# Kernel tuning notes

Measured on AMD Instinct MI355X. Metric: run time of the kernel, lower is better.

## Reference

```python
import jax, jax.numpy as jnp
import numpy as np

H = 12  # num_heads


def rotate_half(x):
    x1, x2 = jnp.split(x, 2, axis=-1)
    return jnp.concatenate([-x2, x1], axis=-1)


def setup_inputs() -> dict:
    key = jax.random.key(0)
    ks = jax.random.split(key, 8)
    B, N, C = 4, 2048, 768
    num_special = 5
    Ns = N - num_special
    D = C // H
    x = jax.random.normal(ks[0], (B, N, C), dtype=jnp.float32)
    rope_cos = jax.random.uniform(ks[1], (Ns, D), dtype=jnp.float32)
    rope_sin = jax.random.uniform(ks[2], (Ns, D), dtype=jnp.float32)
    W_qkv = jax.random.normal(ks[3], (C, 3 * C), dtype=jnp.float32) * (C ** -0.5)
    b_qkv = jax.random.normal(ks[4], (3 * C,), dtype=jnp.float32) * 0.02
    W_proj = jax.random.normal(ks[5], (C, C), dtype=jnp.float32) * (C ** -0.5)
    b_proj = jax.random.normal(ks[6], (C,), dtype=jnp.float32) * 0.02
    return {"x": x, "rope_cos": rope_cos, "rope_sin": rope_sin,
            "W_qkv": W_qkv, "b_qkv": b_qkv, "W_proj": W_proj, "b_proj": b_proj,
            "num_special": num_special}


def reference(x, rope_cos, rope_sin, W_qkv, b_qkv, W_proj, b_proj, num_special):
    B, N, C = x.shape
    D = C // H
    scale = D ** -0.5
    qkv = (x @ W_qkv + b_qkv).reshape(B, N, 3, H, D)
    qkv = jnp.transpose(qkv, (2, 0, 3, 1, 4))  # [3, B, H, N, D]
    q, k, v = qkv[0], qkv[1], qkv[2]
    # partial RoPE: special tokens untouched, spatial tokens rotated
    q_spec, q_spat = q[:, :, :num_special], q[:, :, num_special:]
    k_spec, k_spat = k[:, :, :num_special], k[:, :, num_special:]
    q_spat = q_spat * rope_cos + rotate_half(q_spat) * rope_sin
    k_spat = k_spat * rope_cos + rotate_half(k_spat) * rope_sin
    q = jnp.concatenate([q_spec, q_spat], axis=2)
    k = jnp.concatenate([k_spec, k_spat], axis=2)
    attn = jnp.einsum('bhqd,bhkd->bhqk', q, k) * scale  # [B,H,N,N]
    attn = jax.nn.softmax(attn, axis=-1)
    out = jnp.einsum('bhqk,bhkd->bhqd', attn, v)  # [B,H,N,D]
    out = jnp.transpose(out, (0, 2, 1, 3)).reshape(B, N, C)
    return out @ W_proj + b_proj
```

## Files before the change

### kernel.cpp

```cpp
#include <hip/hip_runtime.h>
#include <stdint.h>

typedef unsigned short u16;
typedef __bf16 bf16x8 __attribute__((ext_vector_type(8)));
typedef __bf16 bf16x2 __attribute__((ext_vector_type(2)));
typedef short s16x4 __attribute__((ext_vector_type(4)));
typedef float f32x4 __attribute__((ext_vector_type(4)));

typedef __attribute__((address_space(1))) void gvoid_t;
typedef __attribute__((address_space(3))) void lvoid_t;

struct alignas(16) U128 { uint32_t x, y, z, w; };
struct alignas(16) F128 { float x, y, z, w; };
struct alignas(8)  U64v { uint32_t x, y; };

__device__ __forceinline__ void gld16(const u16* g, u16* lds) {
  __builtin_amdgcn_global_load_lds((gvoid_t*)const_cast<u16*>(g),
                                   (lvoid_t*)lds, 16, 0, 0);
}

__device__ __forceinline__ u16 f2bf(float f) {
  uint32_t u = __builtin_bit_cast(uint32_t, f);
  u += 0x7FFFu + ((u >> 16) & 1u);
  return (u16)(u >> 16);
}
__device__ __forceinline__ float bf2f(u16 h) {
  return __builtin_bit_cast(float, (uint32_t)h << 16);
}
__device__ __forceinline__ bf16x8 ldfrag(const u16* p) {
  U128 u = *reinterpret_cast<const U128*>(p);
  return __builtin_bit_cast(bf16x8, u);
}
__device__ __forceinline__ uint32_t pkbf(float a, float b) {
  bf16x2 v;
  v[0] = (__bf16)a;
  v[1] = (__bf16)b;
  return __builtin_bit_cast(uint32_t, v);
}

__device__ __forceinline__ float EXP2(float x) { return __builtin_amdgcn_exp2f(x); }

__global__ void cvt_f32_bf16(const float* __restrict__ in, u16* __restrict__ out) {
  int i = (blockIdx.x * 256 + threadIdx.x) * 4;
  F128 v = *reinterpret_cast<const F128*>(in + i);
  U64v o;
  o.x = (uint32_t)f2bf(v.x) | ((uint32_t)f2bf(v.y) << 16);
  o.y = (uint32_t)f2bf(v.z) | ((uint32_t)f2bf(v.w) << 16);
  *reinterpret_cast<U64v*>(out + i) = o;
}

__global__ void transpose_cvt(const float* __restrict__ W, u16* __restrict__ Wt,
                              int K, int N) {
  __shared__ float T[32][33];
  const int n0 = blockIdx.x * 32, k0 = blockIdx.y * 32;
  const int tid = threadIdx.x;
#pragma unroll
  for (int i = 0; i < 4; ++i) {
    int e = i * 256 + tid, r = e >> 5, c = e & 31;
    T[r][c] = W[(size_t)(k0 + r) * N + n0 + c];
  }
  __syncthreads();
#pragma unroll
  for (int i = 0; i < 4; ++i) {
    int e = i * 256 + tid, r = e >> 5, c = e & 31;
    Wt[(size_t)(n0 + r) * K + k0 + c] = f2bf(T[c][r]);
  }
}


#define GEMM_PIPE(A_, Bt_, KD_, NKT_)                                                \
  const int tid = threadIdx.x;                                                       \
  const int wave = tid >> 6, lane = tid & 63;                                        \
  const int quad = lane >> 4, l16 = lane & 15;                                       \
  const int m0 = by * 128, n0 = bx * 128;                                            \
  const int wr = (wave & 1) * 64, wc = (wave >> 1) * 64;                             \
  f32x4 acc[4][4];                                                                   \
  _Pragma("unroll")                                                                  \
  for (int i = 0; i < 4; ++i)                                                        \
    _Pragma("unroll")                                                                \
    for (int j = 0; j < 4; ++j) acc[i][j] = (f32x4){0.f, 0.f, 0.f, 0.f};             \
  const int c0 = wave * 128 + lane;                                                  \
  const int row0 = c0 >> 2, kq0 = c0 & 3;                                            \
  const int c1 = c0 + 64;                                                            \
  const int row1 = c1 >> 2, kq1 = c1 & 3;                                            \
  const u16* Ag0 = (A_) + (size_t)(m0 + row0) * (KD_) + kq0 * 8;                     \
  const u16* Ag1 = (A_) + (size_t)(m0 + row1) * (KD_) + kq1 * 8;                     \
  const u16* Bg0 = (Bt_) + (size_t)(n0 + row0) * (KD_) + kq0 * 8;                    \
  const u16* Bg1 = (Bt_) + (size_t)(n0 + row1) * (KD_) + kq1 * 8;                    \
  STG(0, 0);                                                                         \
  STG(1, 1);                                                                         \
  for (int t = 0; t < (NKT_); ++t) {                                                 \
    __builtin_amdgcn_sched_barrier(0);                                               \
    if (t < (NKT_) - 1) asm volatile("s_waitcnt vmcnt(4)" ::: "memory");             \
    else                asm volatile("s_waitcnt vmcnt(0)" ::: "memory");             \
    __builtin_amdgcn_sched_barrier(0);                                               \
    __builtin_amdgcn_s_barrier();                                                    \
    __builtin_amdgcn_sched_barrier(0);                                               \
    if (t + 2 < (NKT_)) STG(t + 2, (t + 2) % 3);                                     \
    const u16* Ab = Asl + (t % 3) * 4096;                                            \
    const u16* Bb = Bsl + (t % 3) * 4096;                                            \
    bf16x8 af[4], bfr[4];                                                            \
    _Pragma("unroll")                                                                \
    for (int rb = 0; rb < 4; ++rb)                                                   \
      af[rb] = ldfrag(&Ab[(wr + rb * 16 + l16) * 32 + quad * 8]);                    \
    _Pragma("unroll")                                                                \
    for (int cb = 0; cb < 4; ++cb)                                                   \
      bfr[cb] = ldfrag(&Bb[(wc + cb * 16 + l16) * 32 + quad * 8]);                   \
    __builtin_amdgcn_s_setprio(1);                                                   \
    _Pragma("unroll")                                                                \
    for (int rb = 0; rb < 4; ++rb)                                                   \
      _Pragma("unroll")                                                              \
      for (int cb = 0; cb < 4; ++cb)                                                 \
        acc[rb][cb] = __builtin_amdgcn_mfma_f32_16x16x32_bf16(                       \
            af[rb], bfr[cb], acc[rb][cb], 0, 0, 0);                                  \
    __builtin_amdgcn_s_setprio(0);                                                   \
  }

#define STG(t_, s_)                                                                  \
  do {                                                                               \
    const int k0_ = (t_) * 32;                                                       \
    gld16(Ag0 + k0_, &Asl[(s_) * 4096 + wave * 1024]);                               \
    gld16(Bg0 + k0_, &Bsl[(s_) * 4096 + wave * 1024]);                               \
    gld16(Ag1 + k0_, &Asl[(s_) * 4096 + wave * 1024 + 512]);                         \
    gld16(Bg1 + k0_, &Bsl[(s_) * 4096 + wave * 1024 + 512]);                         \
  } while (0)

__global__ __launch_bounds__(256, 3)
void gemm_bt(const u16* __restrict__ A, const u16* __restrict__ Bt,
             const float* __restrict__ bias, float* __restrict__ C,
             int M, int N, int Karg) {
  (void)M; (void)Karg;
  __shared__ u16 Asl[3 * 4096];
  __shared__ u16 Bsl[3 * 4096];
  const int orig = blockIdx.y * 6 + blockIdx.x;
  const int swz = (orig % 8) * 48 + orig / 8;
  const int bx = swz % 6, by = swz / 6;
  GEMM_PIPE(A, Bt, 768, 24)
#pragma unroll
  for (int cb = 0; cb < 4; ++cb) {
    int col = n0 + wc + cb * 16 + l16;
    float bv = bias[col];
#pragma unroll
    for (int rb = 0; rb < 4; ++rb) {
#pragma unroll
      for (int r = 0; r < 4; ++r) {
        int row = m0 + wr + rb * 16 + quad * 4 + r;
        C[(size_t)row * N + col] = acc[rb][cb][r] + bv;
      }
    }
  }
}

__global__ __launch_bounds__(256, 3)
void gemm_qkv_rope(const u16* __restrict__ A, const u16* __restrict__ Bt,
                   const float* __restrict__ bias,
                   const float* __restrict__ cosT, const float* __restrict__ sinT,
                   const int* __restrict__ nsp,
                   u16* __restrict__ Qo, u16* __restrict__ Ko, u16* __restrict__ Vto) {
  __shared__ u16 Asl[3 * 4096];
  __shared__ u16 Bsl[3 * 4096];
  const int orig = blockIdx.y * 18 + blockIdx.x;
  const int swz = (orig % 8) * 144 + orig / 8;
  const int bx = swz % 18, by = swz / 18;
  GEMM_PIPE(A, Bt, 768, 24)

  const int sec = bx / 6;
  const int gcol0 = n0 + wc;
  const int hh = (gcol0 >> 6) % 12;
  const int bb = m0 >> 11;
  const int nbase = m0 & 2047;
  const int bh = bb * 12 + hh;
  const int num_special = nsp[0];
  const float QS = 0.125f * 1.4426950408889634f;

  if (sec < 2) {
    u16* outp = sec ? Ko : Qo;
    const float qs = sec ? 1.0f : QS;
#pragma unroll
    for (int cbp = 0; cbp < 2; ++cbp) {
      const int d1 = cbp * 16 + l16;
      const int d2 = d1 + 32;
      const float bv1 = bias[gcol0 + d1];
      const float bv2 = bias[gcol0 + d2];
#pragma unroll
      for (int rb = 0; rb < 4; ++rb) {
#pragma unroll
        for (int r = 0; r < 4; ++r) {
          const int n = nbase + wr + rb * 16 + quad * 4 + r;
          float v1 = acc[rb][cbp][r] + bv1;
          float v2 = acc[rb][cbp + 2][r] + bv2;
          float o1, o2;
          if (n < num_special) {
            o1 = v1; o2 = v2;
          } else {
            int ns = n - num_special;
            float c1 = cosT[ns * 64 + d1], s1 = sinT[ns * 64 + d1];
            float c2 = cosT[ns * 64 + d2], s2 = sinT[ns * 64 + d2];
            o1 = v1 * c1 - v2 * s1;
            o2 = v2 * c2 + v1 * s2;
          }
          size_t ob = ((size_t)bh * 2048 + n) * 64;
          outp[ob + d1] = f2bf(o1 * qs);
          outp[ob + d2] = f2bf(o2 * qs);
        }
      }
    }
  } else {
#pragma unroll
    for (int cb = 0; cb < 4; ++cb) {
      const int d = cb * 16 + l16;
      const float bv = bias[gcol0 + d];
#pragma unroll
      for (int rb = 0; rb < 4; ++rb) {
        const int nr = nbase + wr + rb * 16 + quad * 4;
        U64v o;
        o.x = (uint32_t)f2bf(acc[rb][cb][0] + bv) |
              ((uint32_t)f2bf(acc[rb][cb][1] + bv) << 16);
        o.y = (uint32_t)f2bf(acc[rb][cb][2] + bv) |
              ((uint32_t)f2bf(acc[rb][cb][3] + bv) << 16);
        *(U64v*)&Vto[((size_t)bh * 64 + d) * 2048 + nr] = o;
      }
    }
  }
}

__global__ __launch_bounds__(256, 3)
void attn(const u16* __restrict__ Q, const u16* __restrict__ Kg,
          const u16* __restrict__ Vt, u16* __restrict__ Out, int qt0) {
  __shared__ u16 smem2[2 * 8192];
  __shared__ float invS[64];
  const int tid = threadIdx.x;
  const int wave = tid >> 6, lane = tid & 63;
  const int quad = lane >> 4, l16 = lane & 15;
  const int idx = blockIdx.x;
  const int bh = idx % 48, qt = idx / 48 + qt0;
  const int b = bh / 12, h = bh % 12;
  const u16* Qb = Q + (size_t)bh * 2048 * 64;
  const u16* Kb = Kg + (size_t)bh * 2048 * 64;
  const u16* Vb = Vt + (size_t)bh * 64 * 2048;
  const int wkey0 = wave * 16;

  const int lrow = lane >> 3;
  const int lch  = (lane & 7) ^ (lrow & 7);
  const int r0a = wave * 8;
  const int r0b = 32 + wave * 8;
  const int ksrc_a = (r0a + lrow) * 64 + lch * 8;
  const int ksrc_b = (r0b + lrow) * 64 + lch * 8;
  const size_t vsrc_a = (size_t)(r0a + lrow) * 2048 + lch * 8;
  const size_t vsrc_b = (size_t)(r0b + lrow) * 2048 + lch * 8;

  const int krd = (wkey0 + l16) * 64 + ((quad ^ (l16 & 7)) << 3);
  int vrd[4];
#pragma unroll
  for (int db = 0; db < 4; ++db)
    vrd[db] = (db * 16 + l16) * 64 +
              ((((wave << 1) | (quad >> 1)) ^ (l16 & 7)) << 3) + (quad & 1) * 4;

#define STAGE_A(kt_, s_)                                                      \
  do {                                                                        \
    u16* Kd = smem2 + (s_) * 8192;                                            \
    u16* Vd = Kd + 4096;                                                      \
    const u16* Ksrc = Kb + (size_t)(kt_) * 4096;                              \
    const u16* Vsrc = Vb + (kt_) * 64;                                        \
    gld16(Ksrc + ksrc_a, Kd + r0a * 64);                                      \
    gld16(Ksrc + ksrc_b, Kd + r0b * 64);                                      \
    gld16(Vsrc + vsrc_a, Vd + r0a * 64);                                      \
    gld16(Vsrc + vsrc_b, Vd + r0b * 64);                                      \
  } while (0)

  bf16x8 qf[4][2];
#pragma unroll
  for (int m = 0; m < 4; ++m) {
    const u16* qp = Qb + (size_t)(qt * 64 + m * 16 + l16) * 64 + quad * 8;
    qf[m][0] = ldfrag(qp);
    qf[m][1] = ldfrag(qp + 32);
  }

  f32x4 oacc[4][4];
#pragma unroll
  for (int m = 0; m < 4; ++m)
#pragma unroll
    for (int db = 0; db < 4; ++db) oacc[m][db] = (f32x4){0.f, 0.f, 0.f, 0.f};
  float psum[4] = {0.f, 0.f, 0.f, 0.f};

  STAGE_A(0, 0);
  STAGE_A(1, 1);
  __syncthreads();

  s16x4 pf[4];
  U64v  vfc[4];
  {
    const u16* Ksh = smem2;
    const u16* Vsh = smem2 + 4096;
    bf16x8 ka0 = ldfrag(Ksh + krd);
    bf16x8 ka1 = ldfrag(Ksh + (krd ^ 32));
#pragma unroll
    for (int db = 0; db < 4; ++db) vfc[db] = *(const U64v*)(Vsh + vrd[db]);
#pragma unroll
    for (int m = 0; m < 4; ++m) {
      f32x4 st = (f32x4){0.f, 0.f, 0.f, 0.f};
      st = __builtin_amdgcn_mfma_f32_16x16x32_bf16(ka0, qf[m][0], st, 0, 0, 0);
      st = __builtin_amdgcn_mfma_f32_16x16x32_bf16(ka1, qf[m][1], st, 0, 0, 0);
      float p0 = EXP2(st[0]), p1 = EXP2(st[1]), p2 = EXP2(st[2]), p3 = EXP2(st[3]);
      psum[m] += (p0 + p1) + (p2 + p3);
      U64v pd; pd.x = pkbf(p0, p1); pd.y = pkbf(p2, p3);
      pf[m] = __builtin_bit_cast(s16x4, pd);
    }
  }
  __syncthreads();

  for (int kt = 0; kt < 31; ++kt) {
    const int cur = kt & 1, nxt = cur ^ 1;
    const u16* Kshn = smem2 + nxt * 8192;
    const u16* Vshn = Kshn + 4096;
    bf16x8 kn0 = ldfrag(Kshn + krd);
    bf16x8 kn1 = ldfrag(Kshn + (krd ^ 32));
    U64v vfn[4];
#pragma unroll
    for (int db = 0; db < 4; ++db) vfn[db] = *(const U64v*)(Vshn + vrd[db]);

    if (kt < 30) STAGE_A(kt + 2, cur);

    s16x4 pfn[4];
#pragma unroll
    for (int m = 0; m < 4; ++m) {
      f32x4 st = (f32x4){0.f, 0.f, 0.f, 0.f};
      st = __builtin_amdgcn_mfma_f32_16x16x32_bf16(kn0, qf[m][0], st, 0, 0, 0);
      st = __builtin_amdgcn_mfma_f32_16x16x32_bf16(kn1, qf[m][1], st, 0, 0, 0);
#pragma unroll
      for (int db = 0; db < 4; ++db)
        oacc[m][db] = __builtin_amdgcn_mfma_f32_16x16x16bf16_1k(pf[m], __builtin_bit_cast(s16x4, vfc[db]), oacc[m][db], 0, 0, 0);
      float p0 = EXP2(st[0]), p1 = EXP2(st[1]), p2 = EXP2(st[2]), p3 = EXP2(st[3]);
      psum[m] += (p0 + p1) + (p2 + p3);
      U64v pd; pd.x = pkbf(p0, p1); pd.y = pkbf(p2, p3);
      pfn[m] = __builtin_bit_cast(s16x4, pd);
    }
    __syncthreads();
#pragma unroll
    for (int m = 0; m < 4; ++m) pf[m] = pfn[m];
#pragma unroll
    for (int db = 0; db < 4; ++db) vfc[db] = vfn[db];
  }

#pragma unroll
  for (int m = 0; m < 4; ++m)
#pragma unroll
    for (int db = 0; db < 4; ++db)
      oacc[m][db] = __builtin_amdgcn_mfma_f32_16x16x16bf16_1k(pf[m], __builtin_bit_cast(s16x4, vfc[db]), oacc[m][db], 0, 0, 0);
#undef STAGE_A

#pragma unroll
  for (int m = 0; m < 4; ++m) {
    psum[m] += __shfl_xor(psum[m], 16, 64);
    psum[m] += __shfl_xor(psum[m], 32, 64);
  }
  __syncthreads();
  float* LS = (float*)smem2;
  if (quad == 0) {
#pragma unroll
    for (int m = 0; m < 4; ++m) LS[wave * 64 + m * 16 + l16] = psum[m];
  }
  __syncthreads();
  if (tid < 64) {
    float tot = LS[tid] + LS[64 + tid] + LS[128 + tid] + LS[192 + tid];
    invS[tid] = 1.0f / tot;
  }

  float* OR = (float*)smem2;
  const int q = tid >> 2;
  const int d0 = (tid & 3) * 4;
  const size_t obase = ((size_t)(b * 2048 + qt * 64 + q)) * 768 + h * 64 + d0;
#pragma unroll
  for (int db = 0; db < 4; ++db) {
    __syncthreads();
#pragma unroll
    for (int m = 0; m < 4; ++m)
#pragma unroll
      for (int r = 0; r < 4; ++r)
        OR[(wave * 64 + m * 16 + quad * 4 + r) * 18 + l16] = oacc[m][db][r];
    __syncthreads();
    float s0 = 0.f, s1 = 0.f, s2 = 0.f, s3 = 0.f;
#pragma unroll
    for (int w = 0; w < 4; ++w) {
      const float* p = &OR[(w * 64 + q) * 18 + d0];
      s0 += p[0]; s1 += p[1]; s2 += p[2]; s3 += p[3];
    }
    float iv = invS[q];
    U64v o;
    o.x = (uint32_t)f2bf(s0 * iv) | ((uint32_t)f2bf(s1 * iv) << 16);
    o.y = (uint32_t)f2bf(s2 * iv) | ((uint32_t)f2bf(s3 * iv) << 16);
    *(U64v*)&Out[obase + db * 16] = o;
  }
}

extern "C" void kernel_launch(void* const* d_in, const int* in_sizes, int n_in,
                              void* d_out, int out_size, void* d_ws, size_t ws_size,
                              hipStream_t stream) {
  (void)in_sizes; (void)n_in; (void)out_size; (void)ws_size;
  const float* x        = (const float*)d_in[0];
  const float* rope_cos = (const float*)d_in[1];
  const float* rope_sin = (const float*)d_in[2];
  const float* W_qkv    = (const float*)d_in[3];
  const float* b_qkv    = (const float*)d_in[4];
  const float* W_proj   = (const float*)d_in[5];
  const float* b_proj   = (const float*)d_in[6];
  const int*   nsp      = (const int*)d_in[7];
  float* out = (float*)d_out;

  char* ws = (char*)d_ws;
  u16* Xb   = (u16*)(ws);
  u16* Wqkt = (u16*)(ws + 12582912);
  u16* Wpt  = (u16*)(ws + 16121856);
  u16* Qb   = (u16*)(ws + 55050240);
  u16* Kb   = (u16*)(ws + 67633152);
  u16* Vtb  = (u16*)(ws + 80216064);
  u16* att  = (u16*)(ws + 92798976);

  cvt_f32_bf16<<<6144, 256, 0, stream>>>(x, Xb);
  transpose_cvt<<<dim3(72, 24), 256, 0, stream>>>(W_qkv, Wqkt, 768, 2304);
  transpose_cvt<<<dim3(24, 24), 256, 0, stream>>>(W_proj, Wpt, 768, 768);
  gemm_qkv_rope<<<dim3(18, 64), 256, 0, stream>>>(Xb, Wqkt, b_qkv, rope_cos, rope_sin,
                                                  nsp, Qb, Kb, Vtb);
  attn<<<768, 256, 0, stream>>>(Qb, Kb, Vtb, att, 0);
  attn<<<768, 256, 0, stream>>>(Qb, Kb, Vtb, att, 16);
  gemm_bt<<<dim3(6, 64), 256, 0, stream>>>(att, Wpt, b_proj, out, 8192, 768, 768);
}
```

Measured before the change: 248.9 us.

## Pair key tiles so PV uses 16x16x32 MFMA and merge attention launches

The attention loop now processes two 64-key tiles per iteration and concatenates their P and V fragments, so the PV product uses the wider 16x16x32 bf16 MFMA instead of two 16x16x16 ones. This halves the PV MFMA instruction count. It also changes software pipelining, since PV for a pair is issued after both QK tiles, and holds more fragments in registers. The two attention launches are merged into one grid of 1536 blocks, removing a launch and a tail.

Measured after the change: 368.1 us. 1.48x slower.

```diff
diff --git a/kernel.cpp b/kernel.cpp
--- a/kernel.cpp
+++ b/kernel.cpp
@@ -29,6 +29,10 @@
 }
 __device__ __forceinline__ bf16x8 ldfrag(const u16* p) {
   U128 u = *reinterpret_cast<const U128*>(p);
+  return __builtin_bit_cast(bf16x8, u);
+}
+__device__ __forceinline__ bf16x8 cat8(U64v lo, U64v hi) {
+  U128 u; u.x = lo.x; u.y = lo.y; u.z = hi.x; u.w = hi.y;
   return __builtin_bit_cast(bf16x8, u);
 }
 __device__ __forceinline__ uint32_t pkbf(float a, float b) {
@@ -226,14 +230,14 @@
 
 __global__ __launch_bounds__(256, 3)
 void attn(const u16* __restrict__ Q, const u16* __restrict__ Kg,
-          const u16* __restrict__ Vt, u16* __restrict__ Out, int qt0) {
+          const u16* __restrict__ Vt, u16* __restrict__ Out) {
   __shared__ u16 smem2[2 * 8192];
   __shared__ float invS[64];
   const int tid = threadIdx.x;
   const int wave = tid >> 6, lane = tid & 63;
   const int quad = lane >> 4, l16 = lane & 15;
   const int idx = blockIdx.x;
-  const int bh = idx % 48, qt = idx / 48 + qt0;
+  const int bh = idx % 48, qt = idx / 48;
   const int b = bh / 12, h = bh % 12;
   const u16* Qb = Q + (size_t)bh * 2048 * 64;
   const u16* Kb = Kg + (size_t)bh * 2048 * 64;
@@ -268,6 +272,25 @@
     gld16(Vsrc + vsrc_b, Vd + r0b * 64);                                      \
   } while (0)
 
+#define QK_TILE(Ksh_, Vsh_, pf_, vdst_)                                       \
+  do {                                                                        \
+    bf16x8 ka0_ = ldfrag((Ksh_) + krd);                                       \
+    bf16x8 ka1_ = ldfrag((Ksh_) + (krd ^ 32));                                \
+    _Pragma("unroll")                                                         \
+    for (int db = 0; db < 4; ++db)                                            \
+      (vdst_)[db] = *(const U64v*)((Vsh_) + vrd[db]);                         \
+    _Pragma("unroll")                                                         \
+    for (int m = 0; m < 4; ++m) {                                             \
+      f32x4 st = (f32x4){0.f, 0.f, 0.f, 0.f};                                 \
+      st = __builtin_amdgcn_mfma_f32_16x16x32_bf16(ka0_, qf[m][0], st, 0, 0, 0); \
+      st = __builtin_amdgcn_mfma_f32_16x16x32_bf16(ka1_, qf[m][1], st, 0, 0, 0); \
+      float p0 = EXP2(st[0]), p1 = EXP2(st[1]), p2 = EXP2(st[2]), p3 = EXP2(st[3]); \
+      psum[m] += (p0 + p1) + (p2 + p3);                                       \
+      U64v pd_; pd_.x = pkbf(p0, p1); pd_.y = pkbf(p2, p3);                   \
+      (pf_)[m] = pd_;                                                         \
+    }                                                                         \
+  } while (0)
+
   bf16x8 qf[4][2];
 #pragma unroll
   for (int m = 0; m < 4; ++m) {
@@ -283,71 +306,56 @@
     for (int db = 0; db < 4; ++db) oacc[m][db] = (f32x4){0.f, 0.f, 0.f, 0.f};
   float psum[4] = {0.f, 0.f, 0.f, 0.f};
 
+  U64v pfE[4], pfO[4], vE[4], vO[4];
+
   STAGE_A(0, 0);
   STAGE_A(1, 1);
   __syncthreads();
-
-  s16x4 pf[4];
-  U64v  vfc[4];
+  QK_TILE(smem2, smem2 + 4096, pfE, vE);
+  __syncthreads();
+
+  for (int j = 0; j < 15; ++j) {
+    {
+      const u16* Ksh = smem2 + 8192;
+      STAGE_A(2 * j + 2, 0);
+      QK_TILE(Ksh, Ksh + 4096, pfO, vO);
+      __syncthreads();
+    }
+    {
+      const u16* Ksh = smem2;
+      U64v pfN[4], vN[4];
+      STAGE_A(2 * j + 3, 1);
+      QK_TILE(Ksh, Ksh + 4096, pfN, vN);
+#pragma unroll
+      for (int db = 0; db < 4; ++db) {
+        bf16x8 vf8 = cat8(vE[db], vO[db]);
+#pragma unroll
+        for (int m = 0; m < 4; ++m)
+          oacc[m][db] = __builtin_amdgcn_mfma_f32_16x16x32_bf16(
+              cat8(pfE[m], pfO[m]), vf8, oacc[m][db], 0, 0, 0);
+      }
+      __syncthreads();
+#pragma unroll
+      for (int m = 0; m < 4; ++m) pfE[m] = pfN[m];
+#pragma unroll
+      for (int db = 0; db < 4; ++db) vE[db] = vN[db];
+    }
+  }
+
   {
-    const u16* Ksh = smem2;
-    const u16* Vsh = smem2 + 4096;
-    bf16x8 ka0 = ldfrag(Ksh + krd);
-    bf16x8 ka1 = ldfrag(Ksh + (krd ^ 32));
-#pragma unroll
-    for (int db = 0; db < 4; ++db) vfc[db] = *(const U64v*)(Vsh + vrd[db]);
-#pragma unroll
-    for (int m = 0; m < 4; ++m) {
-      f32x4 st = (f32x4){0.f, 0.f, 0.f, 0.f};
-      st = __builtin_amdgcn_mfma_f32_16x16x32_bf16(ka0, qf[m][0], st, 0, 0, 0);
-      st = __builtin_amdgcn_mfma_f32_16x16x32_bf16(ka1, qf[m][1], st, 0, 0, 0);
-      float p0 = EXP2(st[0]), p1 = EXP2(st[1]), p2 = EXP2(st[2]), p3 = EXP2(st[3]);
-      psum[m] += (p0 + p1) + (p2 + p3);
-      U64v pd; pd.x = pkbf(p0, p1); pd.y = pkbf(p2, p3);
-      pf[m] = __builtin_bit_cast(s16x4, pd);
-    }
-  }
-  __syncthreads();
-
-  for (int kt = 0; kt < 31; ++kt) {
-    const int cur = kt & 1, nxt = cur ^ 1;
-    const u16* Kshn = smem2 + nxt * 8192;
-    const u16* Vshn = Kshn + 4096;
-    bf16x8 kn0 = ldfrag(Kshn + krd);
-    bf16x8 kn1 = ldfrag(Kshn + (krd ^ 32));
-    U64v vfn[4];
-#pragma unroll
-    for (int db = 0; db < 4; ++db) vfn[db] = *(const U64v*)(Vshn + vrd[db]);
-
-    if (kt < 30) STAGE_A(kt + 2, cur);
-
-    s16x4 pfn[4];
-#pragma unroll
-    for (int m = 0; m < 4; ++m) {
-      f32x4 st = (f32x4){0.f, 0.f, 0.f, 0.f};
-      st = __builtin_amdgcn_mfma_f32_16x16x32_bf16(kn0, qf[m][0], st, 0, 0, 0);
-      st = __builtin_amdgcn_mfma_f32_16x16x32_bf16(kn1, qf[m][1], st, 0, 0, 0);
-#pragma unroll
-      for (int db = 0; db < 4; ++db)
-        oacc[m][db] = __builtin_amdgcn_mfma_f32_16x16x16bf16_1k(pf[m], __builtin_bit_cast(s16x4, vfc[db]), oacc[m][db], 0, 0, 0);
-      float p0 = EXP2(st[0]), p1 = EXP2(st[1]), p2 = EXP2(st[2]), p3 = EXP2(st[3]);
-      psum[m] += (p0 + p1) + (p2 + p3);
-      U64v pd; pd.x = pkbf(p0, p1); pd.y = pkbf(p2, p3);
-      pfn[m] = __builtin_bit_cast(s16x4, pd);
-    }
-    __syncthreads();
-#pragma unroll
-    for (int m = 0; m < 4; ++m) pf[m] = pfn[m];
-#pragma unroll
-    for (int db = 0; db < 4; ++db) vfc[db] = vfn[db];
-  }
-
-#pragma unroll
-  for (int m = 0; m < 4; ++m)
-#pragma unroll
-    for (int db = 0; db < 4; ++db)
-      oacc[m][db] = __builtin_amdgcn_mfma_f32_16x16x16bf16_1k(pf[m], __builtin_bit_cast(s16x4, vfc[db]), oacc[m][db], 0, 0, 0);
+    const u16* Ksh = smem2 + 8192;
+    QK_TILE(Ksh, Ksh + 4096, pfO, vO);
+  }
+#pragma unroll
+  for (int db = 0; db < 4; ++db) {
+    bf16x8 vf8 = cat8(vE[db], vO[db]);
+#pragma unroll
+    for (int m = 0; m < 4; ++m)
+      oacc[m][db] = __builtin_amdgcn_mfma_f32_16x16x32_bf16(
+          cat8(pfE[m], pfO[m]), vf8, oacc[m][db], 0, 0, 0);
+  }
 #undef STAGE_A
+#undef QK_TILE
 
 #pragma unroll
   for (int m = 0; m < 4; ++m) {
@@ -421,7 +429,6 @@
   transpose_cvt<<<dim3(24, 24), 256, 0, stream>>>(W_proj, Wpt, 768, 768);
   gemm_qkv_rope<<<dim3(18, 64), 256, 0, stream>>>(Xb, Wqkt, b_qkv, rope_cos, rope_sin,
                                                   nsp, Qb, Kb, Vtb);
-  attn<<<768, 256, 0, stream>>>(Qb, Kb, Vtb, att, 0);
-  attn<<<768, 256, 0, stream>>>(Qb, Kb, Vtb, att, 16);
+  attn<<<1536, 256, 0, stream>>>(Qb, Kb, Vtb, att);
   gemm_bt<<<dim3(6, 64), 256, 0, stream>>>(att, Wpt, b_proj, out, 8192, 768, 768);
 }
```
